# Performance work log

Measured on AMD Instinct MI355X. Metric: run time of the kernel, lower is better.

The kernel has to match this reference:

```python
import jax, jax.numpy as jnp
import numpy as np

B, C, N = 8, 256, 1024
D, DK, DV, H, NB = 256, 16, 32, 8, 4
P = N + 1


def layernorm(x, g, b, eps=1e-5):
    m = x.mean(-1, keepdims=True)
    v = x.var(-1, keepdims=True)
    return (x - m) / jnp.sqrt(v + eps) * g + b


def bn_inf(x, g, b, mean, var, eps=1e-5):
    # x: [B, C', N]; stats over channel dim
    scale = (g / jnp.sqrt(var + eps))[None, :, None]
    shift = (b - mean * g / jnp.sqrt(var + eps))[None, :, None]
    return x * scale + shift


def softmax_with_policy(attn, policy, eps=1e-6):
    # attn: [B,H,P,P], policy: [B,P,1]
    n = attn.shape[-1]
    ap = policy.reshape(policy.shape[0], 1, 1, n)
    eye = jnp.eye(n, dtype=ap.dtype)[None, None]
    ap = ap + (1.0 - ap) * eye
    m = attn.max(-1, keepdims=True)
    e = jnp.exp(attn - m) * ap
    return (e + eps / n) / (e.sum(-1, keepdims=True) + eps)


def setup_inputs() -> dict:
    key = jax.random.key(0)
    ks = jax.random.split(key, 24)
    s = 0.02
    inp = {
        'x': jax.random.normal(ks[0], (B, C, N), jnp.float32),
        'policy': jnp.ones((B, P, 1), jnp.float32),
        'conv1_w': jax.random.normal(ks[1], (D, C), jnp.float32) * s,
        'conv2_w': jax.random.normal(ks[2], (D, D), jnp.float32) * s,
        'bn1_g': jnp.ones((D,), jnp.float32),
        'bn1_b': jnp.zeros((D,), jnp.float32),
        'bn1_m': jax.random.normal(ks[3], (D,), jnp.float32) * s,
        'bn1_v': jax.random.uniform(ks[4], (D,), jnp.float32, 0.5, 1.5),
        'bn2_g': jnp.ones((D,), jnp.float32),
        'bn2_b': jnp.zeros((D,), jnp.float32),
        'bn2_m': jax.random.normal(ks[5], (D,), jnp.float32) * s,
        'bn2_v': jax.random.uniform(ks[6], (D,), jnp.float32, 0.5, 1.5),
        'cls_token': jax.random.normal(ks[7], (D,), jnp.float32),
        'ln1_g': jnp.ones((NB, D), jnp.float32),
        'ln1_b': jnp.zeros((NB, D), jnp.float32),
        'ln2_g': jnp.ones((NB, D), jnp.float32),
        'ln2_b': jnp.zeros((NB, D), jnp.float32),
        'wq': jax.random.normal(ks[8], (NB, H * DK, D), jnp.float32) * np.sqrt(2.0 / (D + DK)).astype(np.float32),
        'wk': jax.random.normal(ks[9], (NB, H * DK, D), jnp.float32) * np.sqrt(2.0 / (D + DK)).astype(np.float32),
        'wv': jax.random.normal(ks[10], (NB, H * DV, D), jnp.float32) * np.sqrt(2.0 / (D + DV)).astype(np.float32),
        'fc_w': jax.random.normal(ks[11], (NB, D, H * DV), jnp.float32) * s,
        'ff_w1': jax.random.normal(ks[12], (NB, 2 * D, D), jnp.float32) * s,
        'ff_b1': jnp.zeros((NB, 2 * D), jnp.float32),
        'ff_w2': jax.random.normal(ks[13], (NB, D, 2 * D), jnp.float32) * s,
        'ff_b2': jnp.zeros((NB, D), jnp.float32),
    }
    return inp


def reference(x, policy, conv1_w, conv2_w, bn1_g, bn1_b, bn1_m, bn1_v,
              bn2_g, bn2_b, bn2_m, bn2_v, cls_token,
              ln1_g, ln1_b, ln2_g, ln2_b, wq, wk, wv, fc_w,
              ff_w1, ff_b1, ff_w2, ff_b2):
    # stem: 1x1 conv + BN(inference) + ReLU, twice. x: [B, C, N]
    h = jax.nn.relu(bn_inf(jnp.einsum('dc,bcn->bdn', conv1_w, x), bn1_g, bn1_b, bn1_m, bn1_v))
    h = jax.nn.relu(bn_inf(jnp.einsum('dc,bcn->bdn', conv2_w, h), bn2_g, bn2_b, bn2_m, bn2_v))
    h = h.transpose(0, 2, 1)  # [B, N, D]
    cls = jnp.broadcast_to(cls_token[None, None, :], (B, 1, D))
    h = jnp.concatenate([cls, h], axis=1)  # [B, P, D]

    scale = 1.0 / np.sqrt(DK).astype(np.float32)
    for i in range(NB):
        # attention
        y = layernorm(h, ln1_g[i], ln1_b[i])
        q = jnp.einsum('bnd,ed->bne', y, wq[i]).reshape(B, P, H, DK).transpose(0, 2, 1, 3)
        k = jnp.einsum('bnd,ed->bne', y, wk[i]).reshape(B, P, H, DK).transpose(0, 2, 1, 3)
        v = jnp.einsum('bnd,ed->bne', y, wv[i]).reshape(B, P, H, DV).transpose(0, 2, 1, 3)
        attn = jnp.einsum('bhlk,bhtk->bhlt', q, k) * scale
        attn = softmax_with_policy(attn, policy)
        o = jnp.einsum('bhlt,bhtv->bhlv', attn, v)  # [B,H,P,DV]
        o = o.transpose(0, 2, 1, 3).reshape(B, P, H * DV)
        h = h + jnp.einsum('bne,de->bnd', o, fc_w[i])
        # feed-forward
        y = layernorm(h, ln2_g[i], ln2_b[i])
        y = jax.nn.gelu(jnp.einsum('bnd,ed->bne', y, ff_w1[i]) + ff_b1[i], approximate=False)
        h = h + jnp.einsum('bne,de->bnd', y, ff_w2[i]) + ff_b2[i]
    return h
```

## Files before the change

### kernel.cpp

```cpp
#include <hip/hip_runtime.h>
#include <stdint.h>


typedef unsigned short u16;
typedef unsigned int   u32;
typedef __bf16 bf16x8 __attribute__((ext_vector_type(8)));
typedef float  f32x4  __attribute__((ext_vector_type(4)));
typedef float  f32x16 __attribute__((ext_vector_type(16)));
typedef u32    u32x4  __attribute__((ext_vector_type(4)));

#define DEV static __device__ __forceinline__

DEV float b2f(u16 h){ u32 u = ((u32)h) << 16; return __builtin_bit_cast(float, u); }
DEV u16 f2b(float f){ u32 u = __builtin_bit_cast(u32, f); u32 r = (u + 0x7fffu + ((u >> 16) & 1u)) >> 16; return (u16)r; }
DEV float gelu_f(float x){ return 0.5f * x * (1.0f + erff(x * 0.7071067811865475f)); }
DEV u32 cvtpk(float lo, float hi){
  u32 w;
  asm("v_cvt_pk_bf16_f32 %0, %1, %2" : "=v"(w) : "v"(lo), "v"(hi));
  return w;
}
DEV float exp2_(float x){ float r; asm("v_exp_f32 %0, %1" : "=v"(r) : "v"(x)); return r; }

typedef void __attribute__((address_space(1)))* gas_t;
typedef void __attribute__((address_space(3)))* las_t;
DEV void cp16(const void* g, void* l){
  __builtin_amdgcn_global_load_lds((gas_t)(uintptr_t)g, (las_t)(uintptr_t)l, 16, 0, 0);
}

struct Seg { const float* src; u16* dst; int n; int period; int dstride; int block0; float scale; };
struct SegPack { Seg s[8]; };

__global__ __launch_bounds__(256) void k_convert(SegPack p){
  int bid = blockIdx.x;
  int si = 0;
  #pragma unroll
  for (int i = 1; i < 8; i++) if (bid >= p.s[i].block0) si = i;
  const Seg sg = p.s[si];
  int e0 = (bid - sg.block0) * 2048 + threadIdx.x * 8;
  #pragma unroll
  for (int k = 0; k < 8; k++){
    int e = e0 + k;
    if (e < sg.n) sg.dst[(e / sg.period) * sg.dstride + (e % sg.period)] = f2b(sg.src[e] * sg.scale);
  }
}

__global__ __launch_bounds__(256) void k_transpose_x(const float* __restrict__ x, u16* __restrict__ xT){
  __shared__ float t[32][33];
  int b = blockIdx.z, ct = blockIdx.y, nt = blockIdx.x;
  int tx = threadIdx.x & 31, ty = threadIdx.x >> 5;
  const float* xp = x + ((size_t)b * 256 + ct * 32) * 1024 + nt * 32;
  #pragma unroll
  for (int k = 0; k < 4; k++) t[ty + 8*k][tx] = xp[(size_t)(ty + 8*k) * 1024 + tx];
  __syncthreads();
  u16* op = xT + ((size_t)b * 1024 + nt * 32) * 256 + ct * 32;
  #pragma unroll
  for (int k = 0; k < 4; k++) op[(size_t)(ty + 8*k) * 256 + tx] = f2b(t[tx][ty + 8*k]);
}

__global__ void k_cls(const float* __restrict__ cls, float* __restrict__ h){
  int d = threadIdx.x;
  #pragma unroll
  for (int b = 0; b < 8; b++) h[(size_t)b * 1025 * 256 + d] = cls[d];
}

__global__ __launch_bounds__(256) void k_ln(const float* __restrict__ h, const float* __restrict__ g,
                                            const float* __restrict__ bt, u16* __restrict__ y){
  int lane = threadIdx.x & 63, wv = threadIdx.x >> 6;
  long t = (long)blockIdx.x * 4 + wv;
  if (t >= 8200) return;
  const float* row = h + t * 256;
  float4 v = *reinterpret_cast<const float4*>(row + lane * 4);
  float s = v.x + v.y + v.z + v.w;
  float q = v.x*v.x + v.y*v.y + v.z*v.z + v.w*v.w;
  #pragma unroll
  for (int o = 32; o > 0; o >>= 1){ s += __shfl_xor(s, o); q += __shfl_xor(q, o); }
  float mean = s * (1.f/256.f);
  float var  = q * (1.f/256.f) - mean * mean;
  float rs = rsqrtf(var + 1e-5f);
  ushort4 ov;
  const float* vp = &v.x;
  u16* o16 = (u16*)&ov;
  #pragma unroll
  for (int j = 0; j < 4; j++){
    int c = lane * 4 + j;
    o16[j] = f2b((vp[j] - mean) * rs * g[c] + bt[c]);
  }
  *reinterpret_cast<ushort4*>(y + t * 256 + lane * 4) = ov;
}

template<int EPI, int BM, int BN>
__global__ __launch_bounds__(256) void k_gemmT(const u16* __restrict__ A, const u16* __restrict__ W,
    int M, int K, int E, float* __restrict__ outF, u16* __restrict__ outB,
    const float* __restrict__ a0, const float* __restrict__ a1,
    const float* __restrict__ a2, const float* __restrict__ a3){
  constexpr int MR = BM / 32, NR = BN / 32;
  __shared__ __align__(16) u16 As[BM * 64];
  __shared__ __align__(16) u16 Bs[BN * 64];
  const int tid = threadIdx.x;
  const int lane = tid & 63, wv = tid >> 6;
  const int wr = wv >> 1, wc = wv & 1;
  const int tM = blockIdx.x * BM, tN = blockIdx.y * BN;
  f32x4 acc[MR][NR];
  #pragma unroll
  for (int m = 0; m < MR; m++)
    #pragma unroll
    for (int n = 0; n < NR; n++)
      #pragma unroll
      for (int j = 0; j < 4; j++) acc[m][n][j] = 0.f;

  const int l8 = lane >> 3, lm = lane & 7;
  for (int k0 = 0; k0 < K; k0 += 64){
    __syncthreads();
    #pragma unroll
    for (int is = 0; is < BM / 32; is++){
      int row = is * 32 + wv * 8 + l8;
      int kg = lm ^ (row & 7);
      int ra = tM + row; ra = ra < M ? ra : M - 1;
      cp16(A + (size_t)ra * K + k0 + kg * 8, As + is * 2048 + wv * 512);
    }
    #pragma unroll
    for (int is = 0; is < BN / 32; is++){
      int row = is * 32 + wv * 8 + l8;
      int kg = lm ^ (row & 7);
      cp16(W + (size_t)(tN + row) * K + k0 + kg * 8, Bs + is * 2048 + wv * 512);
    }
    __syncthreads();
    #pragma unroll
    for (int kk = 0; kk < 2; kk++){
      bf16x8 af[MR], bfv[NR];
      #pragma unroll
      for (int m = 0; m < MR; m++){
        int row = wr * (BM/2) + m * 16 + (lane & 15);
        int kg = (kk * 4 + (lane >> 4)) ^ (row & 7);
        af[m] = *reinterpret_cast<const bf16x8*>(&As[row * 64 + kg * 8]);
      }
      #pragma unroll
      for (int n = 0; n < NR; n++){
        int row = wc * (BN/2) + n * 16 + (lane & 15);
        int kg = (kk * 4 + (lane >> 4)) ^ (row & 7);
        bfv[n] = *reinterpret_cast<const bf16x8*>(&Bs[row * 64 + kg * 8]);
      }
      #pragma unroll
      for (int m = 0; m < MR; m++)
        #pragma unroll
        for (int n = 0; n < NR; n++)
          acc[m][n] = __builtin_amdgcn_mfma_f32_16x16x32_bf16(af[m], bfv[n], acc[m][n], 0, 0, 0);
    }
  }
  #pragma unroll
  for (int n = 0; n < NR; n++){
    const int col = tN + wc * (BN/2) + n * 16 + (lane & 15);
    float scale = 0.f, shift = 0.f, bias = 0.f;
    if (EPI == 1 || EPI == 2){
      float gv = a0[col], bv = a1[col], mv = a2[col], vv = a3[col];
      scale = gv * rsqrtf(vv + 1e-5f);
      shift = bv - mv * scale;
    }
    if (EPI == 4 || EPI == 5) bias = a0[col];
    #pragma unroll
    for (int m = 0; m < MR; m++){
      const int row0 = tM + wr * (BM/2) + m * 16 + ((lane >> 4) << 2);
      #pragma unroll
      for (int j = 0; j < 4; j++){
        int r = row0 + j;
        if (r < M){
          float v = acc[m][n][j];
          if (EPI == 1){ v = v * scale + shift; v = v > 0.f ? v : 0.f; outB[(size_t)r * E + col] = f2b(v); }
          else if (EPI == 2){ v = v * scale + shift; v = v > 0.f ? v : 0.f; outF[(size_t)(r + (r >> 10) + 1) * 256 + col] = v; }
          else if (EPI == 3){ outF[(size_t)r * E + col] += v; }
          else if (EPI == 4){ outB[(size_t)r * E + col] = f2b(gelu_f(v + bias)); }
          else if (EPI == 5){ outF[(size_t)r * E + col] += v + bias; }
          else {
            if (col < 256){
              outB[(size_t)r * 512 + col] = f2b(v);
            } else {
              u16* vt = (u16*)outF;
              int bb = r / 1025, tok = r - bb * 1025;
              int hv = (col - 256) >> 5, dv = (col - 256) & 31;
              vt[((size_t)((bb * 8 + hv) * 32 + dv)) * 1032 + tok] = f2b(v);
            }
          }
        }
      }
    }
  }
}

__global__ __launch_bounds__(256) void k_attn(const u16* __restrict__ qkv,
    const u16* __restrict__ vt, const float* __restrict__ pol, u16* __restrict__ o){
  __shared__ float pol_s[1088];
  __shared__ float oB[3][32][33];
  __shared__ float lsB[3][32];
  const int tid = threadIdx.x;
  const int lane = tid & 63, wv = tid >> 6;
  const int l32 = lane & 31, hi = lane >> 5;
  const int bid = blockIdx.x;
  const int xcd = bid & 7, idx = bid >> 3;
  const int bh = xcd * 8 + idx / 33, qt = idx % 33;
  const int b = bh >> 3, hh = bh & 7;
  const size_t rowbase = (size_t)b * 1025;
  const int qg = qt * 32 + l32;
  const int qr = qg > 1024 ? 1024 : qg;
  const bf16x8 qf = *reinterpret_cast<const bf16x8*>(qkv + (rowbase + qr) * 512 + hh * 16 + hi * 8);
  float sqq = 0.f;
  {
    const bf16x8 kown = *reinterpret_cast<const bf16x8*>(qkv + (rowbase + qr) * 512 + 128 + hh * 16 + hi * 8);
    #pragma unroll
    for (int i = 0; i < 8; i++) sqq += (float)qf[i] * (float)kown[i];
    sqq += __shfl_xor(sqq, 32);
  }
  const u16* vrow = vt + ((size_t)(bh * 32 + l32)) * 1032;
  for (int t = tid; t < 1088; t += 256) pol_s[t] = (t <= 1024) ? pol[rowbase + t] : 0.f;
  __syncthreads();

  float ls = 0.f;
  f32x16 oacc;
  #pragma unroll
  for (int r = 0; r < 16; r++) oacc[r] = 0.f;

  for (int it = 0; it < 5; it++){
    const int jb = (wv + it * 4) * 64;
    #pragma unroll
    for (int sub = 0; sub < 2; sub++){
      const int jb32 = jb + sub * 32;
      int jrow = jb32 + l32; if (jrow > 1024) jrow = 1024;
      const bf16x8 ka = *reinterpret_cast<const bf16x8*>(qkv + (rowbase + jrow) * 512 + 128 + hh * 16 + hi * 8);
      f32x16 fz;
      #pragma unroll
      for (int r = 0; r < 16; r++) fz[r] = 0.f;
      f32x16 st = __builtin_amdgcn_mfma_f32_32x32x16_bf16(ka, qf, fz, 0, 0, 0);
      float e[16];
      float psum = 0.f;
      #pragma unroll
      for (int r = 0; r < 16; r++){
        int jg2 = jb32 + (r & 3) + 8 * (r >> 2) + 4 * hi;
        int jidx = jg2 > 1087 ? 1087 : jg2;
        float ev = exp2_(st[r]) * pol_s[jidx];
        e[r] = ev;
        psum += ev;
      }
      psum += __shfl_xor(psum, 32);
      ls += psum;
      #pragma unroll
      for (int c = 0; c < 2; c++){
        u32 A0 = cvtpk(e[c*8+0], e[c*8+1]);
        u32 A1 = cvtpk(e[c*8+2], e[c*8+3]);
        u32 B0 = cvtpk(e[c*8+4], e[c*8+5]);
        u32 B1 = cvtpk(e[c*8+6], e[c*8+7]);
        u32 pA0 = __shfl_xor(A0, 32), pB0 = __shfl_xor(B0, 32);
        u32 pA1 = __shfl_xor(A1, 32), pB1 = __shfl_xor(B1, 32);
        u32x4 pw;
        pw.x = hi ? pB0 : A0;
        pw.y = hi ? pB1 : A1;
        pw.z = hi ? B0 : pA0;
        pw.w = hi ? B1 : pA1;
        bf16x8 pb = __builtin_bit_cast(bf16x8, pw);
        bf16x8 va = *reinterpret_cast<const bf16x8*>(vrow + jb32 + c * 16 + hi * 8);
        oacc = __builtin_amdgcn_mfma_f32_32x32x16_bf16(va, pb, oacc, 0, 0, 0);
      }
    }
  }
  __syncthreads();
  if (wv > 0){
    lsB[wv-1][l32] = ls;
    #pragma unroll
    for (int r = 0; r < 16; r++) oB[wv-1][l32][(r & 3) + 8 * (r >> 2) + 4 * hi] = oacc[r];
  }
  __syncthreads();
  if (wv == 0 && qg <= 1024){
    float ls_t = ls + lsB[0][l32] + lsB[1][l32] + lsB[2][l32];
    const float ec = (1.f - pol_s[qg]) * exp2_(sqq);
    ls_t += ec;
    const float inv = 1.f / (ls_t + 1e-6f);
    u16* orow = o + (rowbase + qg) * 256 + hh * 32;
    const u16* vq = qkv + (rowbase + qg) * 512 + 256 + hh * 32;
    #pragma unroll
    for (int rq = 0; rq < 4; rq++){
      const int dv0 = 8 * rq + 4 * hi;
      const ushort4 vv4 = *reinterpret_cast<const ushort4*>(vq + dv0);
      const u16* vv = (const u16*)&vv4;
      uint2 wout;
      u32* wp = &wout.x;
      #pragma unroll
      for (int j2 = 0; j2 < 2; j2++){
        const int d0 = dv0 + j2 * 2;
        float v0 = (oacc[rq*4 + j2*2    ] + oB[0][l32][d0    ] + oB[1][l32][d0    ] + oB[2][l32][d0    ] + ec * b2f(vv[j2*2    ])) * inv;
        float v1 = (oacc[rq*4 + j2*2 + 1] + oB[0][l32][d0 + 1] + oB[1][l32][d0 + 1] + oB[2][l32][d0 + 1] + ec * b2f(vv[j2*2 + 1])) * inv;
        wp[j2] = ((u32)f2b(v1) << 16) | (u32)f2b(v0);
      }
      *reinterpret_cast<uint2*>(orow + dv0) = wout;
    }
  }
}

extern "C" void kernel_launch(void* const* d_in, const int* in_sizes, int n_in,
                              void* d_out, int out_size, void* d_ws, size_t ws_size,
                              hipStream_t stream){
  const float* x    = (const float*)d_in[0];
  const float* pol  = (const float*)d_in[1];
  const float* c1w  = (const float*)d_in[2];
  const float* c2w  = (const float*)d_in[3];
  const float* bn1g = (const float*)d_in[4];
  const float* bn1b = (const float*)d_in[5];
  const float* bn1m = (const float*)d_in[6];
  const float* bn1v = (const float*)d_in[7];
  const float* bn2g = (const float*)d_in[8];
  const float* bn2b = (const float*)d_in[9];
  const float* bn2m = (const float*)d_in[10];
  const float* bn2v = (const float*)d_in[11];
  const float* cls  = (const float*)d_in[12];
  const float* ln1g = (const float*)d_in[13];
  const float* ln1b = (const float*)d_in[14];
  const float* ln2g = (const float*)d_in[15];
  const float* ln2b = (const float*)d_in[16];
  const float* wq   = (const float*)d_in[17];
  const float* wk   = (const float*)d_in[18];
  const float* wvp  = (const float*)d_in[19];
  const float* fcw  = (const float*)d_in[20];
  const float* ffw1 = (const float*)d_in[21];
  const float* ffb1 = (const float*)d_in[22];
  const float* ffw2 = (const float*)d_in[23];
  const float* ffb2 = (const float*)d_in[24];
  float* h = (float*)d_out;

  u16* ws   = (u16*)d_ws;
  u16* wc1  = ws;
  u16* wc2  = wc1  + 65536;
  u16* wqkv = wc2  + 65536;
  u16* wfc  = wqkv + 524288;
  u16* wff1 = wfc  + 262144;
  u16* wff2 = wff1 + 524288;
  u16* xT   = wff2 + 524288;
  u16* h1   = xT   + 2097152;
  u16* yb   = h1   + 2097152;
  u16* qkvb = yb   + 2099200;
  u16* ob   = qkvb + 4198400;
  u16* vtb  = ob   + 2099200;
  u16* ub   = qkvb;

  const float QSCALE = 0.25f * 1.4426950408889634f;
  SegPack sp;
  int b0 = 0;
  sp.s[0] = Seg{ c1w,  wc1,          65536,  65536,  0,      b0, 1.f }; b0 += 32;
  sp.s[1] = Seg{ c2w,  wc2,          65536,  65536,  0,      b0, 1.f }; b0 += 32;
  sp.s[2] = Seg{ wq,   wqkv,         131072, 32768,  131072, b0, QSCALE }; b0 += 64;
  sp.s[3] = Seg{ wk,   wqkv + 32768, 131072, 32768,  131072, b0, 1.f }; b0 += 64;
  sp.s[4] = Seg{ wvp,  wqkv + 65536, 262144, 65536,  131072, b0, 1.f }; b0 += 128;
  sp.s[5] = Seg{ fcw,  wfc,          262144, 262144, 0,      b0, 1.f }; b0 += 128;
  sp.s[6] = Seg{ ffw1, wff1,         524288, 524288, 0,      b0, 1.f }; b0 += 256;
  sp.s[7] = Seg{ ffw2, wff2,         524288, 524288, 0,      b0, 1.f }; b0 += 256;

  k_convert<<<b0, 256, 0, stream>>>(sp);
  k_transpose_x<<<dim3(32, 8, 8), 256, 0, stream>>>(x, xT);
  k_cls<<<1, 256, 0, stream>>>(cls, h);
  k_gemmT<1,64,64><<<dim3(128, 4), 256, 0, stream>>>(xT, wc1, 8192, 256, 256, nullptr, h1, bn1g, bn1b, bn1m, bn1v);
  k_gemmT<2,64,64><<<dim3(128, 4), 256, 0, stream>>>(h1, wc2, 8192, 256, 256, h, nullptr, bn2g, bn2b, bn2m, bn2v);
  for (int i = 0; i < 4; i++){
    k_ln<<<2050, 256, 0, stream>>>(h, ln1g + i*256, ln1b + i*256, yb);
    k_gemmT<6,64,128><<<dim3(129, 4), 256, 0, stream>>>(yb, wqkv + i*131072, 8200, 256, 512, (float*)vtb, qkvb,
                                                        nullptr, nullptr, nullptr, nullptr);
    k_attn<<<2112, 256, 0, stream>>>(qkvb, vtb, pol, ob);
    k_gemmT<3,64,64><<<dim3(129, 4), 256, 0, stream>>>(ob, wfc + i*65536, 8200, 256, 256, h, nullptr,
                                                       nullptr, nullptr, nullptr, nullptr);
    k_ln<<<2050, 256, 0, stream>>>(h, ln2g + i*256, ln2b + i*256, yb);
    k_gemmT<4,64,128><<<dim3(129, 4), 256, 0, stream>>>(yb, wff1 + i*131072, 8200, 256, 512, nullptr, ub,
                                                        ffb1 + i*512, nullptr, nullptr, nullptr);
    k_gemmT<5,64,64><<<dim3(129, 4), 256, 0, stream>>>(ub, wff2 + i*131072, 8200, 512, 256, h, nullptr,
                                                       ffb2 + i*256, nullptr, nullptr, nullptr);
  }
}
```

Before: 398.3 us.

## Fuse layernorm into QKV/FF1 GEMMs, add contiguous per-head K layout, fold policy into exp

Removes the standalone layernorm kernel. Each GEMM block now normalizes its 64 rows of h into a swizzled shared-memory A tile before the MFMA loop, which saves a launch and the bf16 y round trip. Each of the 4 column blocks recomputes the same layernorm, which adds redundant reads of h. The QKV epilogue also writes K into a contiguous per-head [bh][tok][16] buffer so attention reads K with better locality. Attention now stores log2(policy) and adds it inside exp2 instead of multiplying afterwards, and it rebalances key tiles across waves.

```diff
diff --git a/kernel.cpp b/kernel.cpp
--- a/kernel.cpp
+++ b/kernel.cpp
@@ -61,31 +61,6 @@
   int d = threadIdx.x;
   #pragma unroll
   for (int b = 0; b < 8; b++) h[(size_t)b * 1025 * 256 + d] = cls[d];
-}
-
-__global__ __launch_bounds__(256) void k_ln(const float* __restrict__ h, const float* __restrict__ g,
-                                            const float* __restrict__ bt, u16* __restrict__ y){
-  int lane = threadIdx.x & 63, wv = threadIdx.x >> 6;
-  long t = (long)blockIdx.x * 4 + wv;
-  if (t >= 8200) return;
-  const float* row = h + t * 256;
-  float4 v = *reinterpret_cast<const float4*>(row + lane * 4);
-  float s = v.x + v.y + v.z + v.w;
-  float q = v.x*v.x + v.y*v.y + v.z*v.z + v.w*v.w;
-  #pragma unroll
-  for (int o = 32; o > 0; o >>= 1){ s += __shfl_xor(s, o); q += __shfl_xor(q, o); }
-  float mean = s * (1.f/256.f);
-  float var  = q * (1.f/256.f) - mean * mean;
-  float rs = rsqrtf(var + 1e-5f);
-  ushort4 ov;
-  const float* vp = &v.x;
-  u16* o16 = (u16*)&ov;
-  #pragma unroll
-  for (int j = 0; j < 4; j++){
-    int c = lane * 4 + j;
-    o16[j] = f2b((vp[j] - mean) * rs * g[c] + bt[c]);
-  }
-  *reinterpret_cast<ushort4*>(y + t * 256 + lane * 4) = ov;
 }
 
 template<int EPI, int BM, int BN>
@@ -156,7 +131,7 @@
       scale = gv * rsqrtf(vv + 1e-5f);
       shift = bv - mv * scale;
     }
-    if (EPI == 4 || EPI == 5) bias = a0[col];
+    if (EPI == 5) bias = a0[col];
     #pragma unroll
     for (int m = 0; m < MR; m++){
       const int row0 = tM + wr * (BM/2) + m * 16 + ((lane >> 4) << 2);
@@ -168,16 +143,119 @@
           if (EPI == 1){ v = v * scale + shift; v = v > 0.f ? v : 0.f; outB[(size_t)r * E + col] = f2b(v); }
           else if (EPI == 2){ v = v * scale + shift; v = v > 0.f ? v : 0.f; outF[(size_t)(r + (r >> 10) + 1) * 256 + col] = v; }
           else if (EPI == 3){ outF[(size_t)r * E + col] += v; }
-          else if (EPI == 4){ outB[(size_t)r * E + col] = f2b(gelu_f(v + bias)); }
-          else if (EPI == 5){ outF[(size_t)r * E + col] += v + bias; }
+          else { outF[(size_t)r * E + col] += v + bias; }
+        }
+      }
+    }
+  }
+}
+
+template<int EPI, int BN>
+__global__ __launch_bounds__(256) void k_lngemm(const float* __restrict__ hA, const u16* __restrict__ W,
+    int M, int E, const float* __restrict__ lg, const float* __restrict__ lb,
+    float* __restrict__ outF, u16* __restrict__ outB, u16* __restrict__ outK,
+    const float* __restrict__ a0){
+  constexpr int NR = BN / 32;
+  __shared__ __align__(16) u16 As[64 * 256];
+  __shared__ __align__(16) u16 Bs[BN * 64];
+  const int tid = threadIdx.x;
+  const int lane = tid & 63, wv = tid >> 6;
+  const int wr = wv >> 1, wc = wv & 1;
+  const int tM = blockIdx.x * 64, tN = blockIdx.y * BN;
+
+  {
+    const float4 g4 = *reinterpret_cast<const float4*>(lg + lane * 4);
+    const float4 b4 = *reinterpret_cast<const float4*>(lb + lane * 4);
+    for (int i = 0; i < 16; i++){
+      const int row = wv * 16 + i;
+      int ra = tM + row; ra = ra < M ? ra : M - 1;
+      float4 v = *reinterpret_cast<const float4*>(hA + (size_t)ra * 256 + lane * 4);
+      float s = v.x + v.y + v.z + v.w;
+      float q = v.x*v.x + v.y*v.y + v.z*v.z + v.w*v.w;
+      #pragma unroll
+      for (int o = 32; o > 0; o >>= 1){ s += __shfl_xor(s, o); q += __shfl_xor(q, o); }
+      float mean = s * (1.f/256.f);
+      float var  = q * (1.f/256.f) - mean * mean;
+      float rs = rsqrtf(var + 1e-5f);
+      ushort4 ov;
+      u16* o16 = (u16*)&ov;
+      const float* vp = &v.x;
+      const float* gp = &g4.x;
+      const float* bp = &b4.x;
+      #pragma unroll
+      for (int j = 0; j < 4; j++) o16[j] = f2b((vp[j] - mean) * rs * gp[j] + bp[j]);
+      const int gI = (lane >> 1) ^ (row & 7);
+      *reinterpret_cast<ushort4*>(&As[row * 256 + gI * 8 + (lane & 1) * 4]) = ov;
+    }
+  }
+
+  f32x4 acc[2][NR];
+  #pragma unroll
+  for (int m = 0; m < 2; m++)
+    #pragma unroll
+    for (int n = 0; n < NR; n++)
+      #pragma unroll
+      for (int j = 0; j < 4; j++) acc[m][n][j] = 0.f;
+
+  const int l8 = lane >> 3, lm = lane & 7;
+  for (int k0 = 0; k0 < 256; k0 += 64){
+    __syncthreads();
+    #pragma unroll
+    for (int is = 0; is < NR; is++){
+      int row = is * 32 + wv * 8 + l8;
+      int kg = lm ^ (row & 7);
+      cp16(W + (size_t)(tN + row) * 256 + k0 + kg * 8, Bs + is * 2048 + wv * 512);
+    }
+    __syncthreads();
+    #pragma unroll
+    for (int kk = 0; kk < 2; kk++){
+      bf16x8 af[2], bfv[NR];
+      #pragma unroll
+      for (int m = 0; m < 2; m++){
+        int row = wr * 32 + m * 16 + (lane & 15);
+        int kg = (kk * 4 + (lane >> 4)) ^ (row & 7);
+        af[m] = *reinterpret_cast<const bf16x8*>(&As[row * 256 + k0 + kg * 8]);
+      }
+      #pragma unroll
+      for (int n = 0; n < NR; n++){
+        int row = wc * (BN/2) + n * 16 + (lane & 15);
+        int kg = (kk * 4 + (lane >> 4)) ^ (row & 7);
+        bfv[n] = *reinterpret_cast<const bf16x8*>(&Bs[row * 64 + kg * 8]);
+      }
+      #pragma unroll
+      for (int m = 0; m < 2; m++)
+        #pragma unroll
+        for (int n = 0; n < NR; n++)
+          acc[m][n] = __builtin_amdgcn_mfma_f32_16x16x32_bf16(af[m], bfv[n], acc[m][n], 0, 0, 0);
+    }
+  }
+  #pragma unroll
+  for (int n = 0; n < NR; n++){
+    const int col = tN + wc * (BN/2) + n * 16 + (lane & 15);
+    float bias = 0.f;
+    if (EPI == 4) bias = a0[col];
+    #pragma unroll
+    for (int m = 0; m < 2; m++){
+      const int row0 = tM + wr * 32 + m * 16 + ((lane >> 4) << 2);
+      #pragma unroll
+      for (int j = 0; j < 4; j++){
+        int r = row0 + j;
+        if (r < M){
+          float v = acc[m][n][j];
+          if (EPI == 4){ outB[(size_t)r * E + col] = f2b(gelu_f(v + bias)); }
           else {
-            if (col < 256){
+            int bb = r / 1025, tok = r - bb * 1025;
+            if (col < 128){
               outB[(size_t)r * 512 + col] = f2b(v);
+            } else if (col < 256){
+              int hk = (col - 128) >> 4, dk = col & 15;
+              outK[((size_t)((bb * 8 + hk) * 1032 + tok)) * 16 + dk] = f2b(v);
             } else {
+              u16 bv = f2b(v);
+              outB[(size_t)r * 512 + col] = bv;
               u16* vt = (u16*)outF;
-              int bb = r / 1025, tok = r - bb * 1025;
               int hv = (col - 256) >> 5, dv = (col - 256) & 31;
-              vt[((size_t)((bb * 8 + hv) * 32 + dv)) * 1032 + tok] = f2b(v);
+              vt[((size_t)((bb * 8 + hv) * 32 + dv)) * 1032 + tok] = bv;
             }
           }
         }
@@ -187,7 +265,8 @@
 }
 
 __global__ __launch_bounds__(256) void k_attn(const u16* __restrict__ qkv,
-    const u16* __restrict__ vt, const float* __restrict__ pol, u16* __restrict__ o){
+    const u16* __restrict__ kb, const u16* __restrict__ vt,
+    const float* __restrict__ pol, u16* __restrict__ o){
   __shared__ float pol_s[1088];
   __shared__ float oB[3][32][33];
   __shared__ float lsB[3][32];
@@ -199,18 +278,22 @@
   const int bh = xcd * 8 + idx / 33, qt = idx % 33;
   const int b = bh >> 3, hh = bh & 7;
   const size_t rowbase = (size_t)b * 1025;
+  const u16* kbh = kb + (size_t)bh * 1032 * 16;
   const int qg = qt * 32 + l32;
   const int qr = qg > 1024 ? 1024 : qg;
   const bf16x8 qf = *reinterpret_cast<const bf16x8*>(qkv + (rowbase + qr) * 512 + hh * 16 + hi * 8);
   float sqq = 0.f;
   {
-    const bf16x8 kown = *reinterpret_cast<const bf16x8*>(qkv + (rowbase + qr) * 512 + 128 + hh * 16 + hi * 8);
+    const bf16x8 kown = *reinterpret_cast<const bf16x8*>(kbh + (size_t)qr * 16 + hi * 8);
     #pragma unroll
     for (int i = 0; i < 8; i++) sqq += (float)qf[i] * (float)kown[i];
     sqq += __shfl_xor(sqq, 32);
   }
   const u16* vrow = vt + ((size_t)(bh * 32 + l32)) * 1032;
-  for (int t = tid; t < 1088; t += 256) pol_s[t] = (t <= 1024) ? pol[rowbase + t] : 0.f;
+  for (int t = tid; t < 1088; t += 256){
+    float p = (t <= 1024) ? pol[rowbase + t] : 0.f;
+    pol_s[t] = (p > 0.f) ? __log2f(p) : -1.0e30f;
+  }
   __syncthreads();
 
   float ls = 0.f;
@@ -218,13 +301,15 @@
   #pragma unroll
   for (int r = 0; r < 16; r++) oacc[r] = 0.f;
 
-  for (int it = 0; it < 5; it++){
-    const int jb = (wv + it * 4) * 64;
+  const int nt = (wv == 0) ? 5 : 4;
+  for (int it = 0; it < nt; it++){
+    const int jt = (it < 4) ? (wv * 4 + it) : 16;
+    const int jb = jt * 64;
     #pragma unroll
     for (int sub = 0; sub < 2; sub++){
       const int jb32 = jb + sub * 32;
       int jrow = jb32 + l32; if (jrow > 1024) jrow = 1024;
-      const bf16x8 ka = *reinterpret_cast<const bf16x8*>(qkv + (rowbase + jrow) * 512 + 128 + hh * 16 + hi * 8);
+      const bf16x8 ka = *reinterpret_cast<const bf16x8*>(kbh + (size_t)jrow * 16 + hi * 8);
       f32x16 fz;
       #pragma unroll
       for (int r = 0; r < 16; r++) fz[r] = 0.f;
@@ -234,8 +319,7 @@
       #pragma unroll
       for (int r = 0; r < 16; r++){
         int jg2 = jb32 + (r & 3) + 8 * (r >> 2) + 4 * hi;
-        int jidx = jg2 > 1087 ? 1087 : jg2;
-        float ev = exp2_(st[r]) * pol_s[jidx];
+        float ev = exp2_(st[r] + pol_s[jg2]);
         e[r] = ev;
         psum += ev;
       }
@@ -269,7 +353,8 @@
   __syncthreads();
   if (wv == 0 && qg <= 1024){
     float ls_t = ls + lsB[0][l32] + lsB[1][l32] + lsB[2][l32];
-    const float ec = (1.f - pol_s[qg]) * exp2_(sqq);
+    const float pq = exp2_(pol_s[qg]);
+    const float ec = (1.f - pq) * exp2_(sqq);
     ls_t += ec;
     const float inv = 1.f / (ls_t + 1e-6f);
     u16* orow = o + (rowbase + qg) * 256 + hh * 32;
@@ -332,10 +417,10 @@
   u16* wff2 = wff1 + 524288;
   u16* xT   = wff2 + 524288;
   u16* h1   = xT   + 2097152;
-  u16* yb   = h1   + 2097152;
-  u16* qkvb = yb   + 2099200;
+  u16* qkvb = h1   + 2097152;
   u16* ob   = qkvb + 4198400;
   u16* vtb  = ob   + 2099200;
+  u16* kbb  = vtb  + 2117632;
   u16* ub   = qkvb;
 
   const float QSCALE = 0.25f * 1.4426950408889634f;
@@ -356,15 +441,15 @@
   k_gemmT<1,64,64><<<dim3(128, 4), 256, 0, stream>>>(xT, wc1, 8192, 256, 256, nullptr, h1, bn1g, bn1b, bn1m, bn1v);
   k_gemmT<2,64,64><<<dim3(128, 4), 256, 0, stream>>>(h1, wc2, 8192, 256, 256, h, nullptr, bn2g, bn2b, bn2m, bn2v);
   for (int i = 0; i < 4; i++){
-    k_ln<<<2050, 256, 0, stream>>>(h, ln1g + i*256, ln1b + i*256, yb);
-    k_gemmT<6,64,128><<<dim3(129, 4), 256, 0, stream>>>(yb, wqkv + i*131072, 8200, 256, 512, (float*)vtb, qkvb,
-                                                        nullptr, nullptr, nullptr, nullptr);
-    k_attn<<<2112, 256, 0, stream>>>(qkvb, vtb, pol, ob);
+    k_lngemm<6,128><<<dim3(129, 4), 256, 0, stream>>>(h, wqkv + i*131072, 8200, 512,
+                                                      ln1g + i*256, ln1b + i*256,
+                                                      (float*)vtb, qkvb, kbb, nullptr);
+    k_attn<<<2112, 256, 0, stream>>>(qkvb, kbb, vtb, pol, ob);
     k_gemmT<3,64,64><<<dim3(129, 4), 256, 0, stream>>>(ob, wfc + i*65536, 8200, 256, 256, h, nullptr,
                                                        nullptr, nullptr, nullptr, nullptr);
-    k_ln<<<2050, 256, 0, stream>>>(h, ln2g + i*256, ln2b + i*256, yb);
-    k_gemmT<4,64,128><<<dim3(129, 4), 256, 0, stream>>>(yb, wff1 + i*131072, 8200, 256, 512, nullptr, ub,
-                                                        ffb1 + i*512, nullptr, nullptr, nullptr);
+    k_lngemm<4,128><<<dim3(129, 4), 256, 0, stream>>>(h, wff1 + i*131072, 8200, 512,
+                                                      ln2g + i*256, ln2b + i*256,
+                                                      nullptr, ub, nullptr, ffb1 + i*512);
     k_gemmT<5,64,64><<<dim3(129, 4), 256, 0, stream>>>(ub, wff2 + i*131072, 8200, 512, 256, h, nullptr,
                                                        ffb2 + i*256, nullptr, nullptr, nullptr);
   }
```

Result: slower. 432.0 us (+8.5%).

## Store K in per-head contiguous layout and fold policy into exp as log2

Applied to the files above, without the earlier changes.

The QKV GEMM epilogue now writes K into a separate per-(batch, head) contiguous buffer of 16-element rows, so the attention kernel reads K with dense 32-byte loads instead of strided rows of the packed QKV buffer. The policy is stored as log2 in shared memory and added inside the exponent, removing a multiply and the index clamp. Key tiles are reassigned so each wave walks a contiguous block, with wave 0 taking the tail tile. This adds an extra scattered K write in the GEMM epilogue and a new workspace buffer, and the log2 policy trick assumes non-negative policy values.

```diff
diff --git a/kernel.cpp b/kernel.cpp
--- a/kernel.cpp
+++ b/kernel.cpp
@@ -91,6 +91,7 @@
 template<int EPI, int BM, int BN>
 __global__ __launch_bounds__(256) void k_gemmT(const u16* __restrict__ A, const u16* __restrict__ W,
     int M, int K, int E, float* __restrict__ outF, u16* __restrict__ outB,
+    u16* __restrict__ outK,
     const float* __restrict__ a0, const float* __restrict__ a1,
     const float* __restrict__ a2, const float* __restrict__ a3){
   constexpr int MR = BM / 32, NR = BN / 32;
@@ -171,13 +172,18 @@
           else if (EPI == 4){ outB[(size_t)r * E + col] = f2b(gelu_f(v + bias)); }
           else if (EPI == 5){ outF[(size_t)r * E + col] += v + bias; }
           else {
-            if (col < 256){
+            int bb = r / 1025, tok = r - bb * 1025;
+            if (col < 128){
               outB[(size_t)r * 512 + col] = f2b(v);
+            } else if (col < 256){
+              int hk = (col - 128) >> 4, dk = col & 15;
+              outK[((size_t)((bb * 8 + hk) * 1032 + tok)) * 16 + dk] = f2b(v);
             } else {
+              u16 bv = f2b(v);
+              outB[(size_t)r * 512 + col] = bv;
               u16* vt = (u16*)outF;
-              int bb = r / 1025, tok = r - bb * 1025;
               int hv = (col - 256) >> 5, dv = (col - 256) & 31;
-              vt[((size_t)((bb * 8 + hv) * 32 + dv)) * 1032 + tok] = f2b(v);
+              vt[((size_t)((bb * 8 + hv) * 32 + dv)) * 1032 + tok] = bv;
             }
           }
         }
@@ -187,7 +193,8 @@
 }
 
 __global__ __launch_bounds__(256) void k_attn(const u16* __restrict__ qkv,
-    const u16* __restrict__ vt, const float* __restrict__ pol, u16* __restrict__ o){
+    const u16* __restrict__ kb, const u16* __restrict__ vt,
+    const float* __restrict__ pol, u16* __restrict__ o){
   __shared__ float pol_s[1088];
   __shared__ float oB[3][32][33];
   __shared__ float lsB[3][32];
@@ -199,18 +206,22 @@
   const int bh = xcd * 8 + idx / 33, qt = idx % 33;
   const int b = bh >> 3, hh = bh & 7;
   const size_t rowbase = (size_t)b * 1025;
+  const u16* kbh = kb + (size_t)bh * 1032 * 16;
   const int qg = qt * 32 + l32;
   const int qr = qg > 1024 ? 1024 : qg;
   const bf16x8 qf = *reinterpret_cast<const bf16x8*>(qkv + (rowbase + qr) * 512 + hh * 16 + hi * 8);
   float sqq = 0.f;
   {
-    const bf16x8 kown = *reinterpret_cast<const bf16x8*>(qkv + (rowbase + qr) * 512 + 128 + hh * 16 + hi * 8);
+    const bf16x8 kown = *reinterpret_cast<const bf16x8*>(kbh + (size_t)qr * 16 + hi * 8);
     #pragma unroll
     for (int i = 0; i < 8; i++) sqq += (float)qf[i] * (float)kown[i];
     sqq += __shfl_xor(sqq, 32);
   }
   const u16* vrow = vt + ((size_t)(bh * 32 + l32)) * 1032;
-  for (int t = tid; t < 1088; t += 256) pol_s[t] = (t <= 1024) ? pol[rowbase + t] : 0.f;
+  for (int t = tid; t < 1088; t += 256){
+    float p = (t <= 1024) ? pol[rowbase + t] : 0.f;
+    pol_s[t] = (p > 0.f) ? __log2f(p) : -1.0e30f;
+  }
   __syncthreads();
 
   float ls = 0.f;
@@ -218,13 +229,15 @@
   #pragma unroll
   for (int r = 0; r < 16; r++) oacc[r] = 0.f;
 
-  for (int it = 0; it < 5; it++){
-    const int jb = (wv + it * 4) * 64;
+  const int nt = (wv == 0) ? 5 : 4;
+  for (int it = 0; it < nt; it++){
+    const int jt = (it < 4) ? (wv * 4 + it) : 16;
+    const int jb = jt * 64;
     #pragma unroll
     for (int sub = 0; sub < 2; sub++){
       const int jb32 = jb + sub * 32;
       int jrow = jb32 + l32; if (jrow > 1024) jrow = 1024;
-      const bf16x8 ka = *reinterpret_cast<const bf16x8*>(qkv + (rowbase + jrow) * 512 + 128 + hh * 16 + hi * 8);
+      const bf16x8 ka = *reinterpret_cast<const bf16x8*>(kbh + (size_t)jrow * 16 + hi * 8);
       f32x16 fz;
       #pragma unroll
       for (int r = 0; r < 16; r++) fz[r] = 0.f;
@@ -234,8 +247,7 @@
       #pragma unroll
       for (int r = 0; r < 16; r++){
         int jg2 = jb32 + (r & 3) + 8 * (r >> 2) + 4 * hi;
-        int jidx = jg2 > 1087 ? 1087 : jg2;
-        float ev = exp2_(st[r]) * pol_s[jidx];
+        float ev = exp2_(st[r] + pol_s[jg2]);
         e[r] = ev;
         psum += ev;
       }
@@ -269,7 +281,8 @@
   __syncthreads();
   if (wv == 0 && qg <= 1024){
     float ls_t = ls + lsB[0][l32] + lsB[1][l32] + lsB[2][l32];
-    const float ec = (1.f - pol_s[qg]) * exp2_(sqq);
+    const float pq = exp2_(pol_s[qg]);
+    const float ec = (1.f - pq) * exp2_(sqq);
     ls_t += ec;
     const float inv = 1.f / (ls_t + 1e-6f);
     u16* orow = o + (rowbase + qg) * 256 + hh * 32;
@@ -336,6 +349,7 @@
   u16* qkvb = yb   + 2099200;
   u16* ob   = qkvb + 4198400;
   u16* vtb  = ob   + 2099200;
+  u16* kbb  = vtb  + 2117632;
   u16* ub   = qkvb;
 
   const float QSCALE = 0.25f * 1.4426950408889634f;
@@ -353,19 +367,22 @@
   k_convert<<<b0, 256, 0, stream>>>(sp);
   k_transpose_x<<<dim3(32, 8, 8), 256, 0, stream>>>(x, xT);
   k_cls<<<1, 256, 0, stream>>>(cls, h);
-  k_gemmT<1,64,64><<<dim3(128, 4), 256, 0, stream>>>(xT, wc1, 8192, 256, 256, nullptr, h1, bn1g, bn1b, bn1m, bn1v);
-  k_gemmT<2,64,64><<<dim3(128, 4), 256, 0, stream>>>(h1, wc2, 8192, 256, 256, h, nullptr, bn2g, bn2b, bn2m, bn2v);
+  k_gemmT<1,64,64><<<dim3(128, 4), 256, 0, stream>>>(xT, wc1, 8192, 256, 256, nullptr, h1, nullptr,
+                                                     bn1g, bn1b, bn1m, bn1v);
+  k_gemmT<2,64,64><<<dim3(128, 4), 256, 0, stream>>>(h1, wc2, 8192, 256, 256, h, nullptr, nullptr,
+                                                     bn2g, bn2b, bn2m, bn2v);
   for (int i = 0; i < 4; i++){
     k_ln<<<2050, 256, 0, stream>>>(h, ln1g + i*256, ln1b + i*256, yb);
-    k_gemmT<6,64,128><<<dim3(129, 4), 256, 0, stream>>>(yb, wqkv + i*131072, 8200, 256, 512, (float*)vtb, qkvb,
+    k_gemmT<6,64,128><<<dim3(129, 4), 256, 0, stream>>>(yb, wqkv + i*131072, 8200, 256, 512,
+                                                        (float*)vtb, qkvb, kbb,
                                                         nullptr, nullptr, nullptr, nullptr);
-    k_attn<<<2112, 256, 0, stream>>>(qkvb, vtb, pol, ob);
-    k_gemmT<3,64,64><<<dim3(129, 4), 256, 0, stream>>>(ob, wfc + i*65536, 8200, 256, 256, h, nullptr,
+    k_attn<<<2112, 256, 0, stream>>>(qkvb, kbb, vtb, pol, ob);
+    k_gemmT<3,64,64><<<dim3(129, 4), 256, 0, stream>>>(ob, wfc + i*65536, 8200, 256, 256, h, nullptr, nullptr,
                                                        nullptr, nullptr, nullptr, nullptr);
     k_ln<<<2050, 256, 0, stream>>>(h, ln2g + i*256, ln2b + i*256, yb);
-    k_gemmT<4,64,128><<<dim3(129, 4), 256, 0, stream>>>(yb, wff1 + i*131072, 8200, 256, 512, nullptr, ub,
+    k_gemmT<4,64,128><<<dim3(129, 4), 256, 0, stream>>>(yb, wff1 + i*131072, 8200, 256, 512, nullptr, ub, nullptr,
                                                         ffb1 + i*512, nullptr, nullptr, nullptr);
-    k_gemmT<5,64,64><<<dim3(129, 4), 256, 0, stream>>>(ub, wff2 + i*131072, 8200, 512, 256, h, nullptr,
+    k_gemmT<5,64,64><<<dim3(129, 4), 256, 0, stream>>>(ub, wff2 + i*131072, 8200, 512, 256, h, nullptr, nullptr,
                                                        ffb2 + i*256, nullptr, nullptr, nullptr);
   }
 }
```

New measurement: 384.1 us. -3.6%, faster.
